# Kernel tuning notes

Measured on AMD Instinct MI355X. Metric: run time of the kernel, lower is better.

Reference implementation:

```python
import jax, jax.numpy as jnp
import numpy as np

B, S, D = 2, 2048, 4096
NH, NKV, HD = 32, 8, 128
NREP = NH // NKV

def setup_inputs() -> dict:
    key = jax.random.key(0)
    ks = jax.random.split(key, 7)
    sd = 0.02
    return {
        "x": jax.random.normal(ks[0], (B, S, D), dtype=jnp.float32),
        "freqs_cos": jnp.cos(jnp.outer(jnp.arange(S, dtype=jnp.float32), 1.0 / (10000.0 ** (jnp.arange(0, HD, 2, dtype=jnp.float32) / HD)))),
        "freqs_sin": jnp.sin(jnp.outer(jnp.arange(S, dtype=jnp.float32), 1.0 / (10000.0 ** (jnp.arange(0, HD, 2, dtype=jnp.float32) / HD)))),
        "wq": jax.random.normal(ks[1], (D, NH * HD), dtype=jnp.float32) * sd,
        "wk": jax.random.normal(ks[2], (D, NKV * HD), dtype=jnp.float32) * sd,
        "wv": jax.random.normal(ks[3], (D, NKV * HD), dtype=jnp.float32) * sd,
        "wo": jax.random.normal(ks[4], (NH * HD, D), dtype=jnp.float32) * sd,
    }

def _rope(t, cos, sin):
    # t: [b, s, h, hd]; cos/sin: [s, hd/2]
    tr = t.reshape(*t.shape[:-1], -1, 2)
    r, i = tr[..., 0], tr[..., 1]
    c = cos[None, :, None, :]
    s = sin[None, :, None, :]
    out_r = r * c - i * s
    out_i = r * s + i * c
    return jnp.stack([out_r, out_i], axis=-1).reshape(t.shape)

def reference(x, freqs_cos, freqs_sin, wq, wk, wv, wo):
    b, s, _ = x.shape
    xq = (x @ wq).reshape(b, s, NH, HD)
    xk = (x @ wk).reshape(b, s, NKV, HD)
    xv = (x @ wv).reshape(b, s, NKV, HD)
    xq = _rope(xq, freqs_cos, freqs_sin)
    xk = _rope(xk, freqs_cos, freqs_sin)
    # GQA via grouped einsum (equivalent to repeat_kv + SDPA)
    q = xq.transpose(0, 2, 1, 3).reshape(b, NKV, NREP, s, HD)  # [b,g,r,s,d]
    k = xk.transpose(0, 2, 1, 3)  # [b,g,t,d]
    v = xv.transpose(0, 2, 1, 3)
    scale = 1.0 / jnp.sqrt(jnp.float32(HD))
    scores = jnp.einsum('bgrsd,bgtd->bgrst', q, k) * scale
    mask = jnp.where(jnp.triu(jnp.ones((s, s), dtype=bool), 1), -jnp.inf, 0.0).astype(scores.dtype)
    probs = jax.nn.softmax(scores + mask, axis=-1)
    out = jnp.einsum('bgrst,bgtd->bgrsd', probs, v)
    out = out.reshape(b, NH, s, HD).transpose(0, 2, 1, 3).reshape(b, s, NH * HD)
    return out @ wo
```

## Files before the change

kernel.cpp:

```cpp
#include <hip/hip_runtime.h>
#include <hip/hip_bf16.h>
#include <math.h>

typedef __bf16 bf16_t;
typedef __bf16 bf16x4 __attribute__((ext_vector_type(4)));
typedef __bf16 bf16x8 __attribute__((ext_vector_type(8)));
typedef float  f32x4  __attribute__((ext_vector_type(4)));

#define B_   2
#define S_   2048
#define D_   4096
#define NH_  32
#define NKV_ 8
#define HD_  128
#define NREP_ 4
#define QKVN 6144

static __device__ __forceinline__ void gload_lds16(const bf16_t* g, bf16_t* l) {
  __builtin_amdgcn_global_load_lds(
      (const __attribute__((address_space(1))) void*)g,
      (__attribute__((address_space(3))) void*)l, 16, 0, 0);
}

__global__ void convert_f32_bf16(const float* __restrict__ in, bf16_t* __restrict__ out,
                                 size_t n8) {
  size_t i = (size_t)blockIdx.x * blockDim.x + threadIdx.x;
  if (i >= n8) return;
  f32x4 a = *(const f32x4*)(in + i * 8);
  f32x4 b = *(const f32x4*)(in + i * 8 + 4);
  bf16x8 o;
  o[0] = (bf16_t)a[0]; o[1] = (bf16_t)a[1]; o[2] = (bf16_t)a[2]; o[3] = (bf16_t)a[3];
  o[4] = (bf16_t)b[0]; o[5] = (bf16_t)b[1]; o[6] = (bf16_t)b[2]; o[7] = (bf16_t)b[3];
  *(bf16x8*)(out + i * 8) = o;
}

__global__ void transpose_convert(const float* __restrict__ in, bf16_t* __restrict__ out,
                                  int R, int C) {
  __shared__ float tile[32][33];
  const int c0 = blockIdx.x * 32, r0 = blockIdx.y * 32;
  const int tc = threadIdx.x & 31, tr = threadIdx.x >> 5;
#pragma unroll
  for (int i = 0; i < 4; i++) {
    int r = tr + i * 8;
    tile[r][tc] = in[(size_t)(r0 + r) * C + c0 + tc];
  }
  __syncthreads();
#pragma unroll
  for (int i = 0; i < 4; i++) {
    int r = tr + i * 8;
    out[(size_t)(c0 + r) * R + r0 + tc] = (bf16_t)tile[tc][r];
  }
}

__global__ void transpose_v(const bf16_t* __restrict__ qkv, bf16_t* __restrict__ out) {
  __shared__ bf16_t tile[32][33];
  const int t0 = blockIdx.x * 32, d0 = blockIdx.y * 32;
  const int bg = blockIdx.z, b = bg / NKV_, g = bg % NKV_;
  const bf16_t* ibase = qkv + (size_t)b * S_ * QKVN + 5120 + g * HD_;
  bf16_t* obase = out + ((size_t)b * NKV_ + g) * (size_t)HD_ * S_;
  const int tc = threadIdx.x & 31, tr = threadIdx.x >> 5;
#pragma unroll
  for (int i = 0; i < 4; i++) {
    int t = t0 + tr + i * 8;
    tile[tr + i * 8][tc] = ibase[(size_t)t * QKVN + d0 + tc];
  }
  __syncthreads();
#pragma unroll
  for (int i = 0; i < 4; i++) {
    int d = d0 + tr + i * 8;
    obase[(size_t)d * S_ + t0 + tc] = tile[tc][tr + i * 8];
  }
}

__global__ void rope_inplace(bf16_t* __restrict__ x, const float* __restrict__ cosT,
                             const float* __restrict__ sinT, int lgh, size_t nchunks) {
  size_t i = (size_t)blockIdx.x * blockDim.x + threadIdx.x;
  if (i >= nchunks) return;
  const int d8 = (int)(i & 15);
  const int h = (int)((i >> 4) & ((1u << lgh) - 1));
  const size_t pos = i >> (4 + lgh);
  const int s = (int)(pos & (S_ - 1));
  bf16_t* p = x + pos * QKVN + h * HD_ + d8 * 8;
  bf16x8 v = *(bf16x8*)p;
  f32x4 c  = *(const f32x4*)(cosT + (size_t)s * 64 + d8 * 4);
  f32x4 sn = *(const f32x4*)(sinT + (size_t)s * 64 + d8 * 4);
  bf16x8 o;
#pragma unroll
  for (int j = 0; j < 4; j++) {
    float re = (float)v[2 * j], im = (float)v[2 * j + 1];
    o[2 * j]     = (bf16_t)(re * c[j] - im * sn[j]);
    o[2 * j + 1] = (bf16_t)(re * sn[j] + im * c[j]);
  }
  *(bf16x8*)p = o;
}

template <typename OutT>
__global__ __launch_bounds__(512, 2) void gemm8p(const bf16_t* __restrict__ Ag,
                                                 const bf16_t* __restrict__ Bg,
                                                 OutT* __restrict__ C,
                                                 int M, int N, int K) {
  extern __shared__ __align__(16) bf16_t lds[];
  const int t = threadIdx.x;
  const int w = t >> 6, l = t & 63;
  const int wm = w >> 2, wn = w & 3;
  const int lr = l & 15, lg = l >> 4;

  const int nbx = gridDim.x;
  const int nwg = nbx * gridDim.y;
  const int bid = blockIdx.y * nbx + blockIdx.x;
  const int cpx = nwg >> 3;
  const int sid = (bid & 7) * cpx + (bid >> 3);
  const int n0 = (sid % nbx) * 256;
  const int m0 = (sid / nbx) * 256;

  const int srow = t >> 3;
  const int colsw = ((t & 7) ^ (srow & 7)) * 8;
  const int xsw = (lr & 7) * 8;

  auto stageA = [&](int db, int k0, int q) {
    gload_lds16(Ag + (size_t)(m0 + q * 64 + srow) * K + k0 + colsw,
                lds + db * 32768 + q * 4096 + t * 8);
  };
  auto stageB = [&](int db, int k0, int q) {
    gload_lds16(Bg + (size_t)(n0 + q * 64 + srow) * K + k0 + colsw,
                lds + db * 32768 + 16384 + q * 4096 + t * 8);
  };

  f32x4 acc[8][4];
  const f32x4 zero = {0.f, 0.f, 0.f, 0.f};
#pragma unroll
  for (int m = 0; m < 8; m++)
#pragma unroll
    for (int n = 0; n < 4; n++) acc[m][n] = zero;

  bf16x8 bfrag[4][2];
  bf16x8 aE[4], aO[4];

  auto readA = [&](bf16x8* dst, const bf16_t* base, int p) {
    const bf16_t* r0 = base + (wm * 128 + (2 * p) * 16 + lr) * 64;
    const bf16_t* r1 = base + (wm * 128 + (2 * p + 1) * 16 + lr) * 64;
    dst[0] = *(const bf16x8*)(r0 + ((lg * 8) ^ xsw));
    dst[1] = *(const bf16x8*)(r0 + ((32 + lg * 8) ^ xsw));
    dst[2] = *(const bf16x8*)(r1 + ((lg * 8) ^ xsw));
    dst[3] = *(const bf16x8*)(r1 + ((32 + lg * 8) ^ xsw));
  };
  auto readB = [&](const bf16_t* pB) {
#pragma unroll
    for (int n = 0; n < 4; n++)
#pragma unroll
      for (int ks = 0; ks < 2; ks++)
        bfrag[n][ks] =
            *(const bf16x8*)(pB + (wn * 64 + n * 16 + lr) * 64 + ((ks * 32 + lg * 8) ^ xsw));
  };
  auto mfmaPhase = [&](int p, const bf16x8* a) {
    __builtin_amdgcn_s_setprio(1);
#pragma unroll
    for (int n = 0; n < 4; n++)
      acc[2 * p][n] = __builtin_amdgcn_mfma_f32_16x16x32_bf16(a[0], bfrag[n][0], acc[2 * p][n], 0, 0, 0);
#pragma unroll
    for (int n = 0; n < 4; n++)
      acc[2 * p + 1][n] = __builtin_amdgcn_mfma_f32_16x16x32_bf16(a[2], bfrag[n][0], acc[2 * p + 1][n], 0, 0, 0);
#pragma unroll
    for (int n = 0; n < 4; n++)
      acc[2 * p][n] = __builtin_amdgcn_mfma_f32_16x16x32_bf16(a[1], bfrag[n][1], acc[2 * p][n], 0, 0, 0);
#pragma unroll
    for (int n = 0; n < 4; n++)
      acc[2 * p + 1][n] = __builtin_amdgcn_mfma_f32_16x16x32_bf16(a[3], bfrag[n][1], acc[2 * p + 1][n], 0, 0, 0);
    __builtin_amdgcn_s_setprio(0);
  };

  const int KT = K >> 6;

#pragma unroll
  for (int q = 0; q < 4; q++) stageA(0, 0, q);
#pragma unroll
  for (int q = 0; q < 4; q++) stageB(0, 0, q);
#pragma unroll
  for (int q = 0; q < 4; q++) stageB(1, 64, q);
  stageA(1, 64, 0);
  stageA(1, 64, 2);
  asm volatile("s_waitcnt vmcnt(6)" ::: "memory");
  __builtin_amdgcn_s_barrier();
  __builtin_amdgcn_sched_barrier(0);
  readA(aE, lds, 0);

  for (int c = 0; c < KT; ++c) {
    const int d = c & 1;
    const bf16_t* pA = lds + d * 32768;
    const bf16_t* pB = pA + 16384;
    const bool st2 = (c + 2) < KT;
    const int k2 = (c + 2) << 6;

    readB(pB);
    readA(aO, pA, 1);
    if (c + 1 < KT) { stageA(1 - d, (c + 1) << 6, 1); stageA(1 - d, (c + 1) << 6, 3); }
    mfmaPhase(0, aE);
    __builtin_amdgcn_s_barrier();
    __builtin_amdgcn_sched_barrier(0);

    readA(aE, pA, 2);
    if (st2) { stageB(d, k2, 0); stageB(d, k2, 1); }
    mfmaPhase(1, aO);
    __builtin_amdgcn_s_barrier();
    __builtin_amdgcn_sched_barrier(0);

    readA(aO, pA, 3);
    if (st2) { stageB(d, k2, 2); stageB(d, k2, 3); }
    mfmaPhase(2, aE);
    if (st2) asm volatile("s_waitcnt vmcnt(4)" ::: "memory");
    else     asm volatile("s_waitcnt vmcnt(0)" ::: "memory");
    __builtin_amdgcn_s_barrier();
    __builtin_amdgcn_sched_barrier(0);

    if (c + 1 < KT) readA(aE, lds + (1 - d) * 32768, 0);
    if (st2) { stageA(d, k2, 0); stageA(d, k2, 2); }
    mfmaPhase(3, aO);
    __builtin_amdgcn_s_barrier();
    __builtin_amdgcn_sched_barrier(0);
  }

#pragma unroll
  for (int m = 0; m < 8; m++)
#pragma unroll
    for (int n = 0; n < 4; n++) {
      const int row = m0 + wm * 128 + m * 16 + lg * 4;
      const int col = n0 + wn * 64 + n * 16 + lr;
#pragma unroll
      for (int r = 0; r < 4; r++) C[(size_t)(row + r) * N + col] = (OutT)acc[m][n][r];
    }
}

#define QBLK 128
#define KVBLK 64
__global__ __launch_bounds__(256, 2) void flash_attn3(const bf16_t* __restrict__ QKV,
                                                      const bf16_t* __restrict__ Vt,
                                                      const float* __restrict__ cosT,
                                                      const float* __restrict__ sinT,
                                                      bf16_t* __restrict__ O) {
  const int pair = blockIdx.x;
  const int h = blockIdx.y, b = blockIdx.z;
  const int g = h >> 2;
  const int t = threadIdx.x, w = t >> 6, l = t & 63;
  const int lr = l & 15, lg = l >> 4;

  __shared__ __align__(16) char lds[49152];
  char* Ks = lds;
  char* Vs = lds + 16384;
  char* Ps = lds + 32768 + w * 4096;

  const float scale = 0.08838834764831845f;
  const int xm = (lr & 7) << 4;

  for (int phase = 0; phase < 2; phase++) {
    const int qtile = phase ? (15 - pair) : pair;
    const int q0 = qtile * QBLK;
    const int wq = q0 + w * 32;

    bf16x8 qreg[2][4];
#pragma unroll
    for (int qt = 0; qt < 2; qt++) {
      const int s = wq + qt * 16 + lr;
#pragma unroll
      for (int kk = 0; kk < 4; kk++) {
        bf16x8 v = *(const bf16x8*)&QKV[((size_t)b * S_ + s) * QKVN +
                                        h * HD_ + kk * 32 + lg * 8];
        f32x4 c4 = *(const f32x4*)(cosT + (size_t)s * 64 + kk * 16 + lg * 4);
        f32x4 s4 = *(const f32x4*)(sinT + (size_t)s * 64 + kk * 16 + lg * 4);
        bf16x8 o;
#pragma unroll
        for (int j = 0; j < 4; j++) {
          float re = (float)v[2 * j], im = (float)v[2 * j + 1];
          o[2 * j]     = (bf16_t)((re * c4[j] - im * s4[j]) * scale);
          o[2 * j + 1] = (bf16_t)((re * s4[j] + im * c4[j]) * scale);
        }
        qreg[qt][kk] = o;
      }
    }

    float mrun[2] = {-INFINITY, -INFINITY};
    float lrun[2] = {0.f, 0.f};
    f32x4 acc[2][8];
    const f32x4 zero = {0.f, 0.f, 0.f, 0.f};
#pragma unroll
    for (int qt = 0; qt < 2; qt++)
#pragma unroll
      for (int d = 0; d < 8; d++) acc[qt][d] = zero;

    const int nkb = (q0 + QBLK) >> 6;
    for (int kb = 0; kb < nkb; kb++) {
      const int t0 = kb * KVBLK;
      __syncthreads();
#pragma unroll
      for (int i = 0; i < 4; i++) {
        const int c = t + i * 256;
        const int row = c >> 4, sl = c & 15;
        bf16x8 kv = *(const bf16x8*)&QKV[((size_t)b * S_ + t0 + row) * QKVN + 4096 +
                                         g * HD_ + sl * 8];
        *(bf16x8*)(Ks + row * 256 + ((sl * 16) ^ ((row & 7) << 4))) = kv;
      }
#pragma unroll
      for (int i = 0; i < 4; i++) {
        const int c = t + i * 256;
        const int row = c >> 3, sl = c & 7;
        bf16x8 vv = *(const bf16x8*)&Vt[(((size_t)b * NKV_ + g) * HD_ + row) * S_ + t0 + sl * 8];
        *(bf16x8*)(Vs + row * 128 + ((sl * 16) ^ ((row & 7) << 4))) = vv;
      }
      __syncthreads();

      if (t0 > wq + 31) continue;

      f32x4 st[4][2];
#pragma unroll
      for (int n = 0; n < 4; n++) { st[n][0] = zero; st[n][1] = zero; }
#pragma unroll
      for (int kk = 0; kk < 4; kk++) {
        const int colb = (kk * 64 + lg * 16) ^ xm;
#pragma unroll
        for (int n = 0; n < 4; n++) {
          const bf16x8 ak = *(const bf16x8*)(Ks + (n * 16 + lr) * 256 + colb);
          st[n][0] = __builtin_amdgcn_mfma_f32_16x16x32_bf16(ak, qreg[0][kk], st[n][0], 0, 0, 0);
          st[n][1] = __builtin_amdgcn_mfma_f32_16x16x32_bf16(ak, qreg[1][kk], st[n][1], 0, 0, 0);
        }
      }

      const bool needmask = (t0 + KVBLK - 1 > wq);
#pragma unroll
      for (int qt = 0; qt < 2; qt++) {
        const int q = wq + qt * 16 + lr;
        if (needmask) {
#pragma unroll
          for (int n = 0; n < 4; n++)
#pragma unroll
            for (int r = 0; r < 4; r++)
              if (t0 + n * 16 + lg * 4 + r > q) st[n][qt][r] = -INFINITY;
        }
        float mx = -INFINITY;
#pragma unroll
        for (int n = 0; n < 4; n++)
#pragma unroll
          for (int r = 0; r < 4; r++) mx = fmaxf(mx, st[n][qt][r]);
        mx = fmaxf(mx, __shfl_xor(mx, 16));
        mx = fmaxf(mx, __shfl_xor(mx, 32));
        const float mnew = fmaxf(mrun[qt], mx);
        const float corr = __expf(mrun[qt] - mnew);
        mrun[qt] = mnew;
        float sum = 0.f;
        bf16x4 pk[4];
#pragma unroll
        for (int n = 0; n < 4; n++) {
#pragma unroll
          for (int r = 0; r < 4; r++) {
            const float p = __expf(st[n][qt][r] - mnew);
            sum += p;
            pk[n][r] = (bf16_t)p;
          }
        }
        sum += __shfl_xor(sum, 16);
        sum += __shfl_xor(sum, 32);
        lrun[qt] = lrun[qt] * corr + sum;
        {
          char* pbase = Ps + (qt * 16 + lr) * 128;
#pragma unroll
          for (int n = 0; n < 4; n++)
            *(bf16x4*)(pbase + ((n * 32 + lg * 8) ^ xm)) = pk[n];
        }
#pragma unroll
        for (int r = 0; r < 4; r++) {
          const float cb = __shfl(corr, lg * 4 + r);
#pragma unroll
          for (int db = 0; db < 8; db++) acc[qt][db][r] *= cb;
        }
      }

#pragma unroll
      for (int kk = 0; kk < 2; kk++) {
        const int colb = (kk * 64 + lg * 16) ^ xm;
        const bf16x8 ap0 = *(const bf16x8*)(Ps + lr * 128 + colb);
        const bf16x8 ap1 = *(const bf16x8*)(Ps + (16 + lr) * 128 + colb);
#pragma unroll
        for (int db = 0; db < 8; db++) {
          const bf16x8 bv = *(const bf16x8*)(Vs + (db * 16 + lr) * 128 + colb);
          acc[0][db] = __builtin_amdgcn_mfma_f32_16x16x32_bf16(ap0, bv, acc[0][db], 0, 0, 0);
          acc[1][db] = __builtin_amdgcn_mfma_f32_16x16x32_bf16(ap1, bv, acc[1][db], 0, 0, 0);
        }
      }
    }

#pragma unroll
    for (int qt = 0; qt < 2; qt++) {
      const float linv = 1.f / lrun[qt];
#pragma unroll
      for (int r = 0; r < 4; r++) {
        const float li = __shfl(linv, lg * 4 + r);
        const int q = wq + qt * 16 + lg * 4 + r;
#pragma unroll
        for (int db = 0; db < 8; db++)
          O[(((size_t)b * S_ + q) * NH_ + h) * HD_ + db * 16 + lr] = (bf16_t)(acc[qt][db][r] * li);
      }
    }
    __syncthreads();
  }
}

extern "C" void kernel_launch(void* const* d_in, const int* in_sizes, int n_in,
                              void* d_out, int out_size, void* d_ws, size_t ws_size,
                              hipStream_t stream) {
  const float* x    = (const float*)d_in[0];
  const float* fcos = (const float*)d_in[1];
  const float* fsin = (const float*)d_in[2];
  const float* wq   = (const float*)d_in[3];
  const float* wk   = (const float*)d_in[4];
  const float* wv   = (const float*)d_in[5];
  const float* wo   = (const float*)d_in[6];
  float* out = (float*)d_out;

  char* ws = (char*)d_ws;
  bf16_t* x_bf   = (bf16_t*)(ws);
  bf16_t* wqkvT  = (bf16_t*)(ws + 33554432);
  bf16_t* qkv    = (bf16_t*)(ws + 83886080);
  bf16_t* vt     = (bf16_t*)(ws + 134217728);
  bf16_t* attn   = (bf16_t*)(ws + 142606336);

  hipFuncSetAttribute(reinterpret_cast<const void*>(gemm8p<bf16_t>),
                      hipFuncAttributeMaxDynamicSharedMemorySize, 131072);
  hipFuncSetAttribute(reinterpret_cast<const void*>(gemm8p<float>),
                      hipFuncAttributeMaxDynamicSharedMemorySize, 131072);

  convert_f32_bf16<<<8192, 256, 0, stream>>>(x, x_bf, (size_t)2097152);
  transpose_convert<<<dim3(128, 128), 256, 0, stream>>>(wq, wqkvT, 4096, 4096);
  transpose_convert<<<dim3(32, 128), 256, 0, stream>>>(wk, wqkvT + (size_t)4096 * 4096, 4096, 1024);
  transpose_convert<<<dim3(32, 128), 256, 0, stream>>>(wv, wqkvT + (size_t)5120 * 4096, 4096, 1024);
  gemm8p<bf16_t><<<dim3(24, 16), 512, 131072, stream>>>(x_bf, wqkvT, qkv, 4096, QKVN, 4096);
  rope_inplace<<<2048, 256, 0, stream>>>(qkv + 4096, fcos, fsin, 3, (size_t)524288);
  transpose_v<<<dim3(64, 4, 16), 256, 0, stream>>>(qkv, vt);
  transpose_convert<<<dim3(128, 128), 256, 0, stream>>>(wo, wqkvT, 4096, 4096);
  flash_attn3<<<dim3(8, 32, 2), 256, 0, stream>>>(qkv, vt, fcos, fsin, attn);
  gemm8p<float><<<dim3(16, 16), 512, 131072, stream>>>(attn, wqkvT, out, 4096, 4096, 4096);
}
```

Before: 512.4 us.

## Prefetch next KV tile into registers and skip softmax rescale when max stable

The attention kernel now loads the next K/V tile into registers while the current tile is being written to shared memory and processed, so global-memory latency overlaps with compute. It also adds a lazy online-softmax update: when no row's new max exceeds the running max by more than 8, the rescale exponent, the shuffles and the accumulator multiplies are skipped. In exchange, register pressure rises from the prefetch buffers, and unnormalised probabilities can reach about e^8 before the bf16 cast and the fp32 sums.

New measurement: 511.0 us. About the same (-0.3%).

```diff
diff --git a/kernel.cpp b/kernel.cpp
--- a/kernel.cpp
+++ b/kernel.cpp
@@ -232,7 +232,7 @@
 
 #define QBLK 128
 #define KVBLK 64
-__global__ __launch_bounds__(256, 2) void flash_attn3(const bf16_t* __restrict__ QKV,
+__global__ __launch_bounds__(256, 2) void flash_attn4(const bf16_t* __restrict__ QKV,
                                                       const bf16_t* __restrict__ Vt,
                                                       const float* __restrict__ cosT,
                                                       const float* __restrict__ sinT,
@@ -251,6 +251,32 @@
   const float scale = 0.08838834764831845f;
   const int xm = (lr & 7) << 4;
 
+  bf16x8 kpre[4], vpre[4];
+  const int krow = t >> 4, ksl = t & 15;
+  const int vrow = t >> 3, vsl = t & 7;
+  auto loadKV = [&](int t0) {
+#pragma unroll
+    for (int i = 0; i < 4; i++)
+      kpre[i] = *(const bf16x8*)&QKV[((size_t)b * S_ + t0 + krow + i * 16) * QKVN + 4096 +
+                                     g * HD_ + ksl * 8];
+#pragma unroll
+    for (int i = 0; i < 4; i++)
+      vpre[i] = *(const bf16x8*)&Vt[(((size_t)b * NKV_ + g) * HD_ + vrow + i * 32) * S_ +
+                                    t0 + vsl * 8];
+  };
+  auto writeKV = [&]() {
+#pragma unroll
+    for (int i = 0; i < 4; i++) {
+      const int row = krow + i * 16;
+      *(bf16x8*)(Ks + row * 256 + ((ksl * 16) ^ ((row & 7) << 4))) = kpre[i];
+    }
+#pragma unroll
+    for (int i = 0; i < 4; i++) {
+      const int row = vrow + i * 32;
+      *(bf16x8*)(Vs + row * 128 + ((vsl * 16) ^ ((row & 7) << 4))) = vpre[i];
+    }
+  };
+
   for (int phase = 0; phase < 2; phase++) {
     const int qtile = phase ? (15 - pair) : pair;
     const int q0 = qtile * QBLK;
@@ -287,24 +313,12 @@
       for (int d = 0; d < 8; d++) acc[qt][d] = zero;
 
     const int nkb = (q0 + QBLK) >> 6;
+    loadKV(0);
     for (int kb = 0; kb < nkb; kb++) {
       const int t0 = kb * KVBLK;
       __syncthreads();
-#pragma unroll
-      for (int i = 0; i < 4; i++) {
-        const int c = t + i * 256;
-        const int row = c >> 4, sl = c & 15;
-        bf16x8 kv = *(const bf16x8*)&QKV[((size_t)b * S_ + t0 + row) * QKVN + 4096 +
-                                         g * HD_ + sl * 8];
-        *(bf16x8*)(Ks + row * 256 + ((sl * 16) ^ ((row & 7) << 4))) = kv;
-      }
-#pragma unroll
-      for (int i = 0; i < 4; i++) {
-        const int c = t + i * 256;
-        const int row = c >> 3, sl = c & 7;
-        bf16x8 vv = *(const bf16x8*)&Vt[(((size_t)b * NKV_ + g) * HD_ + row) * S_ + t0 + sl * 8];
-        *(bf16x8*)(Vs + row * 128 + ((sl * 16) ^ ((row & 7) << 4))) = vv;
-      }
+      writeKV();
+      if (kb + 1 < nkb) loadKV(t0 + KVBLK);
       __syncthreads();
 
       if (t0 > wq + 31) continue;
@@ -341,9 +355,15 @@
           for (int r = 0; r < 4; r++) mx = fmaxf(mx, st[n][qt][r]);
         mx = fmaxf(mx, __shfl_xor(mx, 16));
         mx = fmaxf(mx, __shfl_xor(mx, 32));
-        const float mnew = fmaxf(mrun[qt], mx);
-        const float corr = __expf(mrun[qt] - mnew);
-        mrun[qt] = mnew;
+
+        const bool nore = __all(mx <= mrun[qt] + 8.0f);
+        float mnew, corr;
+        if (nore) {
+          mnew = mrun[qt];
+        } else {
+          mnew = fmaxf(mrun[qt], mx);
+          corr = __expf(mrun[qt] - mnew);
+        }
         float sum = 0.f;
         bf16x4 pk[4];
 #pragma unroll
@@ -357,18 +377,23 @@
         }
         sum += __shfl_xor(sum, 16);
         sum += __shfl_xor(sum, 32);
-        lrun[qt] = lrun[qt] * corr + sum;
+        if (nore) {
+          lrun[qt] += sum;
+        } else {
+          lrun[qt] = lrun[qt] * corr + sum;
+          mrun[qt] = mnew;
+#pragma unroll
+          for (int r = 0; r < 4; r++) {
+            const float cb = __shfl(corr, lg * 4 + r);
+#pragma unroll
+            for (int db = 0; db < 8; db++) acc[qt][db][r] *= cb;
+          }
+        }
         {
           char* pbase = Ps + (qt * 16 + lr) * 128;
 #pragma unroll
           for (int n = 0; n < 4; n++)
             *(bf16x4*)(pbase + ((n * 32 + lg * 8) ^ xm)) = pk[n];
-        }
-#pragma unroll
-        for (int r = 0; r < 4; r++) {
-          const float cb = __shfl(corr, lg * 4 + r);
-#pragma unroll
-          for (int db = 0; db < 8; db++) acc[qt][db][r] *= cb;
         }
       }
 
@@ -434,6 +459,6 @@
   rope_inplace<<<2048, 256, 0, stream>>>(qkv + 4096, fcos, fsin, 3, (size_t)524288);
   transpose_v<<<dim3(64, 4, 16), 256, 0, stream>>>(qkv, vt);
   transpose_convert<<<dim3(128, 128), 256, 0, stream>>>(wo, wqkvT, 4096, 4096);
-  flash_attn3<<<dim3(8, 32, 2), 256, 0, stream>>>(qkv, vt, fcos, fsin, attn);
+  flash_attn4<<<dim3(8, 32, 2), 256, 0, stream>>>(qkv, vt, fcos, fsin, attn);
   gemm8p<float><<<dim3(16, 16), 512, 131072, stream>>>(attn, wqkvT, out, 4096, 4096, 4096);
 }
```
